# Optimization experiments

Measured on AMD Instinct MI355X. Metric: run time of the kernel, lower is better.

Reference implementation:

```python
import jax, jax.numpy as jnp
import numpy as np

N = 8192
NUM_FEAT = 512
NUM_HIDDENS = 128


def _mlp_params(key, fin, fh):
    k1, k2, k3, k4 = jax.random.split(key, 4)
    s1 = 1.0 / np.sqrt(fin)
    s2 = 1.0 / np.sqrt(fh)
    W1 = jax.random.uniform(k1, (fin, fh), jnp.float32, -s1, s1)
    b1 = jax.random.uniform(k2, (fh,), jnp.float32, -s1, s1)
    W2 = jax.random.uniform(k3, (fh, fh), jnp.float32, -s2, s2)
    b2 = jax.random.uniform(k4, (fh,), jnp.float32, -s2, s2)
    return W1, b1, W2, b2


def setup_inputs() -> dict:
    key = jax.random.key(0)
    ks = jax.random.split(key, 9)
    feat = jax.random.normal(ks[0], (N, NUM_FEAT), jnp.float32)
    adj = jax.random.uniform(ks[1], (N, N), jnp.float32)
    aa = jax.random.uniform(ks[2], (N, N), jnp.float32)
    mod = jax.random.normal(ks[3], (N, N), jnp.float32)
    Wl1, bl1, Wl2, bl2 = _mlp_params(ks[4], NUM_FEAT, NUM_HIDDENS)
    Wu1, bu1, Wu2, bu2 = _mlp_params(ks[5], NUM_FEAT, NUM_HIDDENS)
    Wa1, ba1, Wa2, ba2 = _mlp_params(ks[6], NUM_FEAT, NUM_HIDDENS)
    Wm1, bm1, Wm2, bm2 = _mlp_params(ks[7], NUM_FEAT, NUM_HIDDENS)
    ws = jnp.zeros((3,), jnp.float32)  # nn.init.zeros_(weighted_sum)
    return dict(feat=feat, adj=adj, aa=aa, mod=mod,
                Wl1=Wl1, bl1=bl1, Wl2=Wl2, bl2=bl2,
                Wu1=Wu1, bu1=bu1, Wu2=Wu2, bu2=bu2,
                Wa1=Wa1, ba1=ba1, Wa2=Wa2, ba2=ba2,
                Wm1=Wm1, bm1=bm1, Wm2=Wm2, bm2=bm2,
                ws=ws)


def _latent(feat, W1, b1, W2, b2):
    h = jax.nn.relu(feat @ W1 + b1)
    return h @ W2 + b2  # [N, H]


def reference(feat, adj, aa, mod,
              Wl1, bl1, Wl2, bl2,
              Wu1, bu1, Wu2, bu2,
              Wa1, ba1, Wa2, ba2,
              Wm1, bm1, Wm2, bm2, ws):
    lat_link = _latent(feat, Wl1, bl1, Wl2, bl2)
    lat_aa = _latent(feat, Wa1, ba1, Wa2, ba2)
    lat_mod = _latent(feat, Wm1, bm1, Wm2, bm2)
    lat_unlink = _latent(feat, Wu1, bu1, Wu2, bu2)

    link_ctx = jax.nn.sigmoid(lat_link @ lat_link.T)          # [N, N]
    aa_ctx = jax.nn.sigmoid((lat_aa @ lat_aa.T) * aa)         # [N, N]
    mod_ctx = jax.nn.sigmoid((lat_mod @ lat_mod.T) * mod)     # [N, N]

    w = jax.nn.softmax(ws)  # [3]
    # cat(..., dim=2) @ w  ==  weighted sum of the three contexts
    weight_link = w[0] * link_ctx + w[1] * aa_ctx + w[2] * mod_ctx

    weight_unlink = jax.nn.sigmoid(lat_unlink @ lat_unlink.T)
    return (weight_link - weight_unlink) * adj + weight_unlink
```

## Files before the change

kernel.cpp:

```cpp
#include <hip/hip_runtime.h>


typedef __attribute__((ext_vector_type(8))) short short8;
typedef __attribute__((ext_vector_type(4))) float f32x4;

__device__ __forceinline__ unsigned short f2bf(float x) {
  union { float f; unsigned u; } v; v.f = x;
  unsigned u = v.u + 0x7FFFu + ((v.u >> 16) & 1u);
  return (unsigned short)(u >> 16);
}

__device__ __forceinline__ float sigf(float x) {
  float e = __builtin_amdgcn_exp2f(-1.4426950408889634f * x);
  return __builtin_amdgcn_rcpf(1.0f + e);
}

__device__ __forceinline__ void gload_lds16(const float* g, float* l) {
  __builtin_amdgcn_global_load_lds(
      (const __attribute__((address_space(1))) void*)g,
      (__attribute__((address_space(3))) void*)l, 16, 0, 0);
}

__global__ __launch_bounds__(256) void k_featfrag(const float* __restrict__ feat,
                                                  unsigned short* __restrict__ dst) {
  int t = blockIdx.x * 256 + threadIdx.x;
  int row = t >> 6, kc = t & 63;
  const float4* s = reinterpret_cast<const float4*>(feat + row * 512 + kc * 8);
  float4 v0 = s[0], v1 = s[1];
  short8 o;
  o[0] = f2bf(v0.x); o[1] = f2bf(v0.y); o[2] = f2bf(v0.z); o[3] = f2bf(v0.w);
  o[4] = f2bf(v1.x); o[5] = f2bf(v1.y); o[6] = f2bf(v1.z); o[7] = f2bf(v1.w);
  int mb = row >> 4, kk = kc >> 2;
  int lane = ((kc & 3) << 4) | (row & 15);
  *reinterpret_cast<short8*>(dst + ((size_t)((mb * 16 + kk) * 64 + lane)) * 8) = o;
}

__global__ __launch_bounds__(256) void k_wfrag(
    const float* __restrict__ w1_0, const float* __restrict__ w1_1,
    const float* __restrict__ w1_2, const float* __restrict__ w1_3,
    const float* __restrict__ w2_0, const float* __restrict__ w2_1,
    const float* __restrict__ w2_2, const float* __restrict__ w2_3,
    unsigned short* __restrict__ w1f, unsigned short* __restrict__ w2f) {
  int t = blockIdx.x * 256 + threadIdx.x;
  if (t < 32768) {
    int lane = t & 63, nb = (t >> 6) & 7, kk = (t >> 9) & 15, g = t >> 13;
    const float* W = g == 0 ? w1_0 : g == 1 ? w1_1 : g == 2 ? w1_2 : w1_3;
    int q = lane >> 4, r = lane & 15;
    int col = nb * 16 + r;
    short8 o;
#pragma unroll
    for (int j = 0; j < 8; ++j) o[j] = f2bf(W[(kk * 32 + q * 8 + j) * 128 + col]);
    *reinterpret_cast<short8*>(w1f + (size_t)t * 8) = o;
  } else if (t < 40960) {
    int t2 = t - 32768;
    int lane = t2 & 63, nb = (t2 >> 6) & 7, kk = (t2 >> 9) & 3, g = t2 >> 11;
    const float* W = g == 0 ? w2_0 : g == 1 ? w2_1 : g == 2 ? w2_2 : w2_3;
    int q = lane >> 4, r = lane & 15;
    int col = nb * 16 + r;
    short8 o;
#pragma unroll
    for (int j = 0; j < 8; ++j) o[j] = f2bf(W[(kk * 32 + q * 8 + j) * 128 + col]);
    *reinterpret_cast<short8*>(w2f + (size_t)t2 * 8) = o;
  }
}

__global__ __launch_bounds__(256) void k_gemm1(
    const unsigned short* __restrict__ featf, const unsigned short* __restrict__ w1f,
    const float* __restrict__ b1_0, const float* __restrict__ b1_1,
    const float* __restrict__ b1_2, const float* __restrict__ b1_3,
    unsigned short* __restrict__ hfrag) {
  int bi = blockIdx.x, g = blockIdx.y;
  int lane = threadIdx.x & 63, w = threadIdx.x >> 6;
  int wm = w >> 1, wn = w & 1;
  int q = lane >> 4, r = lane & 15;
  int mbase = 8 * bi + 4 * wm;

  f32x4 s[4][4];
#pragma unroll
  for (int mi = 0; mi < 4; ++mi)
#pragma unroll
    for (int nj = 0; nj < 4; ++nj) s[mi][nj] = (f32x4){0.f, 0.f, 0.f, 0.f};

  for (int kk = 0; kk < 16; ++kk) {
    short8 a[4], b[4];
#pragma unroll
    for (int mi = 0; mi < 4; ++mi)
      a[mi] = *reinterpret_cast<const short8*>(
          featf + ((size_t)(((mbase + mi) * 16 + kk) * 64 + lane)) * 8);
#pragma unroll
    for (int nj = 0; nj < 4; ++nj)
      b[nj] = *reinterpret_cast<const short8*>(
          w1f + ((size_t)(((g * 16 + kk) * 8 + 4 * wn + nj) * 64 + lane)) * 8);
#pragma unroll
    for (int mi = 0; mi < 4; ++mi)
#pragma unroll
      for (int nj = 0; nj < 4; ++nj)
        s[mi][nj] = __builtin_amdgcn_mfma_f32_16x16x32_bf16(a[mi], b[nj], s[mi][nj], 0, 0, 0);
  }

  const float* b1 = g == 0 ? b1_0 : g == 1 ? b1_1 : g == 2 ? b1_2 : b1_3;
#pragma unroll
  for (int nj = 0; nj < 4; ++nj) {
    int cl = 64 * wn + 16 * nj + r;
    float bias = b1[cl];
    int Cg = 128 * g + cl;
    int kkd = Cg >> 5;
    int lane2hi = ((Cg >> 3) & 3) << 4;
    int j2 = Cg & 7;
#pragma unroll
    for (int mi = 0; mi < 4; ++mi) {
#pragma unroll
      for (int v = 0; v < 4; ++v) {
        int R = 128 * bi + 64 * wm + 16 * mi + 4 * q + v;
        float val = fmaxf(s[mi][nj][v] + bias, 0.0f);
        int mb = R >> 4;
        int lane2 = lane2hi | (R & 15);
        hfrag[((size_t)((mb * 16 + kkd) * 64 + lane2)) * 8 + j2] = f2bf(val);
      }
    }
  }
}

__global__ __launch_bounds__(256) void k_gemm2(
    const unsigned short* __restrict__ hfrag, const unsigned short* __restrict__ w2f,
    const float* __restrict__ b2_0, const float* __restrict__ b2_1,
    const float* __restrict__ b2_2, const float* __restrict__ b2_3,
    unsigned short* __restrict__ latf) {
  int bi = blockIdx.x, g = blockIdx.y;
  int lane = threadIdx.x & 63, w = threadIdx.x >> 6;
  int wm = w >> 1, wn = w & 1;
  int q = lane >> 4, r = lane & 15;
  int mbase = 8 * bi + 4 * wm;

  f32x4 s[4][4];
#pragma unroll
  for (int mi = 0; mi < 4; ++mi)
#pragma unroll
    for (int nj = 0; nj < 4; ++nj) s[mi][nj] = (f32x4){0.f, 0.f, 0.f, 0.f};

#pragma unroll
  for (int kk = 0; kk < 4; ++kk) {
    short8 a[4], b[4];
#pragma unroll
    for (int mi = 0; mi < 4; ++mi)
      a[mi] = *reinterpret_cast<const short8*>(
          hfrag + ((size_t)(((mbase + mi) * 16 + 4 * g + kk) * 64 + lane)) * 8);
#pragma unroll
    for (int nj = 0; nj < 4; ++nj)
      b[nj] = *reinterpret_cast<const short8*>(
          w2f + ((size_t)(((g * 4 + kk) * 8 + 4 * wn + nj) * 64 + lane)) * 8);
#pragma unroll
    for (int mi = 0; mi < 4; ++mi)
#pragma unroll
      for (int nj = 0; nj < 4; ++nj)
        s[mi][nj] = __builtin_amdgcn_mfma_f32_16x16x32_bf16(a[mi], b[nj], s[mi][nj], 0, 0, 0);
  }

  const float* b2 = g == 0 ? b2_0 : g == 1 ? b2_1 : g == 2 ? b2_2 : b2_3;
#pragma unroll
  for (int nj = 0; nj < 4; ++nj) {
    int cl = 64 * wn + 16 * nj + r;
    float bias = b2[cl];
    int kkd = cl >> 5;
    int lane2hi = ((cl >> 3) & 3) << 4;
    int j2 = cl & 7;
#pragma unroll
    for (int mi = 0; mi < 4; ++mi) {
#pragma unroll
      for (int v = 0; v < 4; ++v) {
        int R = 128 * bi + 64 * wm + 16 * mi + 4 * q + v;
        float val = s[mi][nj][v] + bias;
        int mb = R >> 4;
        int lane2 = lane2hi | (R & 15);
        latf[((size_t)(((g * 512 + mb) * 4 + kkd) * 64 + lane2)) * 8 + j2] = f2bf(val);
      }
    }
  }
}

__global__ __launch_bounds__(256, 3) void k_ctx(
    const unsigned short* __restrict__ latf,
    const float* __restrict__ adj, const float* __restrict__ aa,
    const float* __restrict__ mod, const float* __restrict__ wsv,
    float* __restrict__ out) {
  __shared__ float smem[2][3][4][256];

  int bid = blockIdx.x;
  int colstrip = bid & 7;
  int rowgrp = bid >> 3;

  int tid = threadIdx.x;
  int lane = tid & 63, w = tid >> 6;
  int q = lane >> 4, r = lane & 15;

  int mbi = rowgrp * 4 + w;
  int mbj0 = colstrip * 64;

  size_t ewoff = (size_t)(mbi * 16 + r) * 8192 + (size_t)colstrip * 1024 + 4 * q;

  float s0w = wsv[0], s1w = wsv[1], s2w = wsv[2];
  float mx = fmaxf(fmaxf(s0w, s1w), s2w);
  float e0 = __builtin_amdgcn_exp2f(1.4426950408889634f * (s0w - mx));
  float e1 = __builtin_amdgcn_exp2f(1.4426950408889634f * (s1w - mx));
  float e2 = __builtin_amdgcn_exp2f(1.4426950408889634f * (s2w - mx));
  float inv = __builtin_amdgcn_rcpf(e0 + e1 + e2);
  float w0 = e0 * inv, w1 = e1 * inv, w2 = e2 * inv;

  const size_t GS = (size_t)512 * 2048;

  short8 fi[4][4];
#pragma unroll
  for (int g = 0; g < 4; ++g)
#pragma unroll
    for (int kk = 0; kk < 4; ++kk) {
      fi[g][kk] = *reinterpret_cast<const short8*>(
          latf + GS * g + (((size_t)mbi * 4 + kk) << 9) + lane * 8);
      asm volatile("" : "+v"(fi[g][kk]));
    }

  gload_lds16(aa + ewoff, &smem[0][0][w][0]);
  gload_lds16(mod + ewoff, &smem[0][1][w][0]);
  gload_lds16(adj + ewoff, &smem[0][2][w][0]);
  asm volatile("s_waitcnt vmcnt(0)" ::: "memory");

  for (int t = 0; t < 64; ++t) {
    int buf = t & 1, nbuf = buf ^ 1;
    const unsigned short* fjb =
        latf + (((size_t)(mbj0 + t) * 4) << 9) + lane * 8;

    short8 fj[4][4];
#pragma unroll
    for (int g = 0; g < 4; ++g)
#pragma unroll
      for (int kk = 0; kk < 4; ++kk)
        fj[g][kk] = *reinterpret_cast<const short8*>(fjb + GS * g + 512 * kk);

    __builtin_amdgcn_sched_barrier(0);
    {
      size_t ewnext = ewoff + (size_t)(t < 63 ? t + 1 : t) * 16;
      gload_lds16(aa + ewnext, &smem[nbuf][0][w][0]);
      gload_lds16(mod + ewnext, &smem[nbuf][1][w][0]);
      gload_lds16(adj + ewnext, &smem[nbuf][2][w][0]);
    }
    asm volatile("s_waitcnt vmcnt(3)" ::: "memory");

    f32x4 sg, o4;

    sg = (f32x4){0.f, 0.f, 0.f, 0.f};
    sg = __builtin_amdgcn_mfma_f32_16x16x32_bf16(fj[0][0], fi[0][0], sg, 0, 0, 0);
    sg = __builtin_amdgcn_mfma_f32_16x16x32_bf16(fj[0][1], fi[0][1], sg, 0, 0, 0);
    sg = __builtin_amdgcn_mfma_f32_16x16x32_bf16(fj[0][2], fi[0][2], sg, 0, 0, 0);
    sg = __builtin_amdgcn_mfma_f32_16x16x32_bf16(fj[0][3], fi[0][3], sg, 0, 0, 0);
#pragma unroll
    for (int v = 0; v < 4; ++v) o4[v] = w0 * sigf(sg[v]);

    sg = (f32x4){0.f, 0.f, 0.f, 0.f};
    sg = __builtin_amdgcn_mfma_f32_16x16x32_bf16(fj[1][0], fi[1][0], sg, 0, 0, 0);
    sg = __builtin_amdgcn_mfma_f32_16x16x32_bf16(fj[1][1], fi[1][1], sg, 0, 0, 0);
    sg = __builtin_amdgcn_mfma_f32_16x16x32_bf16(fj[1][2], fi[1][2], sg, 0, 0, 0);
    sg = __builtin_amdgcn_mfma_f32_16x16x32_bf16(fj[1][3], fi[1][3], sg, 0, 0, 0);
    {
      f32x4 ew = *reinterpret_cast<const f32x4*>(&smem[buf][0][w][lane * 4]);
#pragma unroll
      for (int v = 0; v < 4; ++v) o4[v] += w1 * sigf(sg[v] * ew[v]);
    }

    sg = (f32x4){0.f, 0.f, 0.f, 0.f};
    sg = __builtin_amdgcn_mfma_f32_16x16x32_bf16(fj[2][0], fi[2][0], sg, 0, 0, 0);
    sg = __builtin_amdgcn_mfma_f32_16x16x32_bf16(fj[2][1], fi[2][1], sg, 0, 0, 0);
    sg = __builtin_amdgcn_mfma_f32_16x16x32_bf16(fj[2][2], fi[2][2], sg, 0, 0, 0);
    sg = __builtin_amdgcn_mfma_f32_16x16x32_bf16(fj[2][3], fi[2][3], sg, 0, 0, 0);
    {
      f32x4 ew = *reinterpret_cast<const f32x4*>(&smem[buf][1][w][lane * 4]);
#pragma unroll
      for (int v = 0; v < 4; ++v) o4[v] += w2 * sigf(sg[v] * ew[v]);
    }

    sg = (f32x4){0.f, 0.f, 0.f, 0.f};
    sg = __builtin_amdgcn_mfma_f32_16x16x32_bf16(fj[3][0], fi[3][0], sg, 0, 0, 0);
    sg = __builtin_amdgcn_mfma_f32_16x16x32_bf16(fj[3][1], fi[3][1], sg, 0, 0, 0);
    sg = __builtin_amdgcn_mfma_f32_16x16x32_bf16(fj[3][2], fi[3][2], sg, 0, 0, 0);
    sg = __builtin_amdgcn_mfma_f32_16x16x32_bf16(fj[3][3], fi[3][3], sg, 0, 0, 0);
    {
      f32x4 ew = *reinterpret_cast<const f32x4*>(&smem[buf][2][w][lane * 4]);
      f32x4 res;
#pragma unroll
      for (int v = 0; v < 4; ++v) {
        float u = sigf(sg[v]);
        res[v] = ew[v] * (o4[v] - u) + u;
      }
      __builtin_nontemporal_store(res, reinterpret_cast<f32x4*>(out + ewoff + (size_t)t * 16));
    }
  }
}

extern "C" void kernel_launch(void* const* d_in, const int* in_sizes, int n_in,
                              void* d_out, int out_size, void* d_ws, size_t ws_size,
                              hipStream_t stream) {
  const float* feat = (const float*)d_in[0];
  const float* adj  = (const float*)d_in[1];
  const float* aa   = (const float*)d_in[2];
  const float* mod  = (const float*)d_in[3];
  const float* W1g[4] = {(const float*)d_in[4], (const float*)d_in[12],
                         (const float*)d_in[16], (const float*)d_in[8]};
  const float* b1g[4] = {(const float*)d_in[5], (const float*)d_in[13],
                         (const float*)d_in[17], (const float*)d_in[9]};
  const float* W2g[4] = {(const float*)d_in[6], (const float*)d_in[14],
                         (const float*)d_in[18], (const float*)d_in[10]};
  const float* b2g[4] = {(const float*)d_in[7], (const float*)d_in[15],
                         (const float*)d_in[19], (const float*)d_in[11]};
  const float* wsv = (const float*)d_in[20];
  float* out = (float*)d_out;

  unsigned short* featf = (unsigned short*)d_ws;
  unsigned short* hfrag = featf + 4194304;
  unsigned short* latf  = hfrag + 4194304;
  unsigned short* w1f   = latf + 4194304;
  unsigned short* w2f   = w1f + 262144;
  if (ws_size < 25821184) return;

  k_featfrag<<<2048, 256, 0, stream>>>(feat, featf);
  k_wfrag<<<160, 256, 0, stream>>>(W1g[0], W1g[1], W1g[2], W1g[3],
                                   W2g[0], W2g[1], W2g[2], W2g[3], w1f, w2f);
  k_gemm1<<<dim3(64, 4), 256, 0, stream>>>(featf, w1f, b1g[0], b1g[1], b1g[2], b1g[3], hfrag);
  k_gemm2<<<dim3(64, 4), 256, 0, stream>>>(hfrag, w2f, b2g[0], b2g[1], b2g[2], b2g[3], latf);
  k_ctx<<<1024, 256, 0, stream>>>(latf, adj, aa, mod, wsv, out);
}
```

Before: 448.9 us.

## Restructure ctx kernel: one row block per workgroup, share latent fragments via LDS

Each workgroup of 8 waves now handles a full 16-row strip across all columns. The row-side latent fragments are staged once in LDS instead of held in registers per wave, and the elementwise adj/aa/mod tiles are loaded as contiguous 128-column row chunks. Per-step barriers synchronise the double-buffered LDS prefetch. This makes the elementwise reads and output writes full-row contiguous and frees registers, but it adds LDS reads of the fragments every step, a workgroup barrier per iteration, and output stores that are no longer nontemporal.

```diff
diff --git a/kernel.cpp b/kernel.cpp
--- a/kernel.cpp
+++ b/kernel.cpp
@@ -19,6 +19,25 @@
   __builtin_amdgcn_global_load_lds(
       (const __attribute__((address_space(1))) void*)g,
       (__attribute__((address_space(3))) void*)l, 16, 0, 0);
+}
+__device__ __forceinline__ void gload_lds16u(const unsigned short* g, unsigned short* l) {
+  __builtin_amdgcn_global_load_lds(
+      (const __attribute__((address_space(1))) void*)g,
+      (__attribute__((address_space(3))) void*)l, 16, 0, 0);
+}
+
+__device__ __forceinline__ unsigned lds_off(const void* p) {
+  return (unsigned)(uintptr_t)(const __attribute__((address_space(3))) void*)p;
+}
+__device__ __forceinline__ f32x4 ds_read_f32x4(unsigned a) {
+  f32x4 d;
+  asm volatile("ds_read_b128 %0, %1" : "=v"(d) : "v"(a));
+  return d;
+}
+__device__ __forceinline__ short8 ds_read_frag(unsigned a) {
+  short8 d;
+  asm volatile("ds_read_b128 %0, %1" : "=v"(d) : "v"(a));
+  return d;
 }
 
 __global__ __launch_bounds__(256) void k_featfrag(const float* __restrict__ feat,
@@ -178,25 +197,19 @@
   }
 }
 
-__global__ __launch_bounds__(256, 3) void k_ctx(
+__global__ __launch_bounds__(512, 2) void k_ctx(
     const unsigned short* __restrict__ latf,
     const float* __restrict__ adj, const float* __restrict__ aa,
     const float* __restrict__ mod, const float* __restrict__ wsv,
     float* __restrict__ out) {
-  __shared__ float smem[2][3][4][256];
+  __shared__ unsigned short fi_lds[8192];
+  __shared__ float ew_lds[2][3][2048];
 
   int bid = blockIdx.x;
-  int colstrip = bid & 7;
-  int rowgrp = bid >> 3;
-
   int tid = threadIdx.x;
   int lane = tid & 63, w = tid >> 6;
   int q = lane >> 4, r = lane & 15;
-
-  int mbi = rowgrp * 4 + w;
-  int mbj0 = colstrip * 64;
-
-  size_t ewoff = (size_t)(mbi * 16 + r) * 8192 + (size_t)colstrip * 1024 + 4 * q;
+  int mbi = bid;
 
   float s0w = wsv[0], s1w = wsv[1], s2w = wsv[2];
   float mx = fmaxf(fmaxf(s0w, s1w), s2w);
@@ -208,26 +221,31 @@
 
   const size_t GS = (size_t)512 * 2048;
 
-  short8 fi[4][4];
-#pragma unroll
-  for (int g = 0; g < 4; ++g)
-#pragma unroll
-    for (int kk = 0; kk < 4; ++kk) {
-      fi[g][kk] = *reinterpret_cast<const short8*>(
-          latf + GS * g + (((size_t)mbi * 4 + kk) << 9) + lane * 8);
-      asm volatile("" : "+v"(fi[g][kk]));
-    }
-
-  gload_lds16(aa + ewoff, &smem[0][0][w][0]);
-  gload_lds16(mod + ewoff, &smem[0][1][w][0]);
-  gload_lds16(adj + ewoff, &smem[0][2][w][0]);
+#pragma unroll
+  for (int e = 0; e < 2; ++e) {
+    int i = 2 * w + e;
+    int g = i >> 2, kk = i & 3;
+    gload_lds16u(latf + GS * g + (size_t)(mbi * 4 + kk) * 512 + lane * 8,
+                 &fi_lds[i * 512]);
+  }
+  size_t rowbase = (size_t)(mbi * 16 + 2 * w + (lane >> 5)) * 8192 + (lane & 31) * 4;
+  gload_lds16(aa + rowbase, &ew_lds[0][0][w * 256]);
+  gload_lds16(mod + rowbase, &ew_lds[0][1][w * 256]);
+  gload_lds16(adj + rowbase, &ew_lds[0][2][w * 256]);
   asm volatile("s_waitcnt vmcnt(0)" ::: "memory");
-
-  for (int t = 0; t < 64; ++t) {
-    int buf = t & 1, nbuf = buf ^ 1;
+  __builtin_amdgcn_s_barrier();
+
+  unsigned fib = lds_off(fi_lds);
+  unsigned ewb = lds_off(&ew_lds[0][0][0]);
+  unsigned l16 = (unsigned)lane * 16u;
+  unsigned ewlane = (unsigned)(((r >> 1) * 256 + (r & 1) * 128 + 16 * w + 4 * q) * 4);
+
+#pragma unroll 1
+  for (int s = 0; s < 64; ++s) {
+    int buf = s & 1, nbuf = buf ^ 1;
+
     const unsigned short* fjb =
-        latf + (((size_t)(mbj0 + t) * 4) << 9) + lane * 8;
-
+        latf + (size_t)((s * 8 + w) * 4) * 512 + lane * 8;
     short8 fj[4][4];
 #pragma unroll
     for (int g = 0; g < 4; ++g)
@@ -236,61 +254,97 @@
         fj[g][kk] = *reinterpret_cast<const short8*>(fjb + GS * g + 512 * kk);
 
     __builtin_amdgcn_sched_barrier(0);
-    {
-      size_t ewnext = ewoff + (size_t)(t < 63 ? t + 1 : t) * 16;
-      gload_lds16(aa + ewnext, &smem[nbuf][0][w][0]);
-      gload_lds16(mod + ewnext, &smem[nbuf][1][w][0]);
-      gload_lds16(adj + ewnext, &smem[nbuf][2][w][0]);
-    }
+
+    {
+      int s1 = (s < 63) ? s + 1 : s;
+      size_t fs = rowbase + (size_t)s1 * 128;
+      gload_lds16(aa + fs, &ew_lds[nbuf][0][w * 256]);
+      gload_lds16(mod + fs, &ew_lds[nbuf][1][w * 256]);
+      gload_lds16(adj + fs, &ew_lds[nbuf][2][w * 256]);
+    }
+    __builtin_amdgcn_sched_barrier(0);
     asm volatile("s_waitcnt vmcnt(3)" ::: "memory");
+    __builtin_amdgcn_sched_barrier(0);
+
+    unsigned ewc = ewb + (unsigned)buf * 24576u + ewlane;
+    f32x4 ewa = ds_read_f32x4(ewc);
+    f32x4 ewm = ds_read_f32x4(ewc + 8192u);
+    f32x4 ewj = ds_read_f32x4(ewc + 16384u);
 
     f32x4 sg, o4;
 
-    sg = (f32x4){0.f, 0.f, 0.f, 0.f};
-    sg = __builtin_amdgcn_mfma_f32_16x16x32_bf16(fj[0][0], fi[0][0], sg, 0, 0, 0);
-    sg = __builtin_amdgcn_mfma_f32_16x16x32_bf16(fj[0][1], fi[0][1], sg, 0, 0, 0);
-    sg = __builtin_amdgcn_mfma_f32_16x16x32_bf16(fj[0][2], fi[0][2], sg, 0, 0, 0);
-    sg = __builtin_amdgcn_mfma_f32_16x16x32_bf16(fj[0][3], fi[0][3], sg, 0, 0, 0);
-#pragma unroll
-    for (int v = 0; v < 4; ++v) o4[v] = w0 * sigf(sg[v]);
-
-    sg = (f32x4){0.f, 0.f, 0.f, 0.f};
-    sg = __builtin_amdgcn_mfma_f32_16x16x32_bf16(fj[1][0], fi[1][0], sg, 0, 0, 0);
-    sg = __builtin_amdgcn_mfma_f32_16x16x32_bf16(fj[1][1], fi[1][1], sg, 0, 0, 0);
-    sg = __builtin_amdgcn_mfma_f32_16x16x32_bf16(fj[1][2], fi[1][2], sg, 0, 0, 0);
-    sg = __builtin_amdgcn_mfma_f32_16x16x32_bf16(fj[1][3], fi[1][3], sg, 0, 0, 0);
-    {
-      f32x4 ew = *reinterpret_cast<const f32x4*>(&smem[buf][0][w][lane * 4]);
-#pragma unroll
-      for (int v = 0; v < 4; ++v) o4[v] += w1 * sigf(sg[v] * ew[v]);
-    }
-
-    sg = (f32x4){0.f, 0.f, 0.f, 0.f};
-    sg = __builtin_amdgcn_mfma_f32_16x16x32_bf16(fj[2][0], fi[2][0], sg, 0, 0, 0);
-    sg = __builtin_amdgcn_mfma_f32_16x16x32_bf16(fj[2][1], fi[2][1], sg, 0, 0, 0);
-    sg = __builtin_amdgcn_mfma_f32_16x16x32_bf16(fj[2][2], fi[2][2], sg, 0, 0, 0);
-    sg = __builtin_amdgcn_mfma_f32_16x16x32_bf16(fj[2][3], fi[2][3], sg, 0, 0, 0);
-    {
-      f32x4 ew = *reinterpret_cast<const f32x4*>(&smem[buf][1][w][lane * 4]);
-#pragma unroll
-      for (int v = 0; v < 4; ++v) o4[v] += w2 * sigf(sg[v] * ew[v]);
-    }
-
-    sg = (f32x4){0.f, 0.f, 0.f, 0.f};
-    sg = __builtin_amdgcn_mfma_f32_16x16x32_bf16(fj[3][0], fi[3][0], sg, 0, 0, 0);
-    sg = __builtin_amdgcn_mfma_f32_16x16x32_bf16(fj[3][1], fi[3][1], sg, 0, 0, 0);
-    sg = __builtin_amdgcn_mfma_f32_16x16x32_bf16(fj[3][2], fi[3][2], sg, 0, 0, 0);
-    sg = __builtin_amdgcn_mfma_f32_16x16x32_bf16(fj[3][3], fi[3][3], sg, 0, 0, 0);
-    {
-      f32x4 ew = *reinterpret_cast<const f32x4*>(&smem[buf][2][w][lane * 4]);
+    {
+      short8 f0 = ds_read_frag(fib + 0 * 1024 + l16);
+      short8 f1 = ds_read_frag(fib + 1 * 1024 + l16);
+      short8 f2 = ds_read_frag(fib + 2 * 1024 + l16);
+      short8 f3 = ds_read_frag(fib + 3 * 1024 + l16);
+      asm volatile("s_waitcnt lgkmcnt(0)" ::: "memory");
+      __builtin_amdgcn_sched_barrier(0);
+      sg = (f32x4){0.f, 0.f, 0.f, 0.f};
+      sg = __builtin_amdgcn_mfma_f32_16x16x32_bf16(fj[0][0], f0, sg, 0, 0, 0);
+      sg = __builtin_amdgcn_mfma_f32_16x16x32_bf16(fj[0][1], f1, sg, 0, 0, 0);
+      sg = __builtin_amdgcn_mfma_f32_16x16x32_bf16(fj[0][2], f2, sg, 0, 0, 0);
+      sg = __builtin_amdgcn_mfma_f32_16x16x32_bf16(fj[0][3], f3, sg, 0, 0, 0);
+#pragma unroll
+      for (int v = 0; v < 4; ++v) o4[v] = w0 * sigf(sg[v]);
+    }
+
+    {
+      short8 f0 = ds_read_frag(fib + 4 * 1024 + l16);
+      short8 f1 = ds_read_frag(fib + 5 * 1024 + l16);
+      short8 f2 = ds_read_frag(fib + 6 * 1024 + l16);
+      short8 f3 = ds_read_frag(fib + 7 * 1024 + l16);
+      asm volatile("s_waitcnt lgkmcnt(0)" ::: "memory");
+      __builtin_amdgcn_sched_barrier(0);
+      sg = (f32x4){0.f, 0.f, 0.f, 0.f};
+      sg = __builtin_amdgcn_mfma_f32_16x16x32_bf16(fj[1][0], f0, sg, 0, 0, 0);
+      sg = __builtin_amdgcn_mfma_f32_16x16x32_bf16(fj[1][1], f1, sg, 0, 0, 0);
+      sg = __builtin_amdgcn_mfma_f32_16x16x32_bf16(fj[1][2], f2, sg, 0, 0, 0);
+      sg = __builtin_amdgcn_mfma_f32_16x16x32_bf16(fj[1][3], f3, sg, 0, 0, 0);
+#pragma unroll
+      for (int v = 0; v < 4; ++v) o4[v] += w1 * sigf(sg[v] * ewa[v]);
+    }
+
+    {
+      short8 f0 = ds_read_frag(fib + 8 * 1024 + l16);
+      short8 f1 = ds_read_frag(fib + 9 * 1024 + l16);
+      short8 f2 = ds_read_frag(fib + 10 * 1024 + l16);
+      short8 f3 = ds_read_frag(fib + 11 * 1024 + l16);
+      asm volatile("s_waitcnt lgkmcnt(0)" ::: "memory");
+      __builtin_amdgcn_sched_barrier(0);
+      sg = (f32x4){0.f, 0.f, 0.f, 0.f};
+      sg = __builtin_amdgcn_mfma_f32_16x16x32_bf16(fj[2][0], f0, sg, 0, 0, 0);
+      sg = __builtin_amdgcn_mfma_f32_16x16x32_bf16(fj[2][1], f1, sg, 0, 0, 0);
+      sg = __builtin_amdgcn_mfma_f32_16x16x32_bf16(fj[2][2], f2, sg, 0, 0, 0);
+      sg = __builtin_amdgcn_mfma_f32_16x16x32_bf16(fj[2][3], f3, sg, 0, 0, 0);
+#pragma unroll
+      for (int v = 0; v < 4; ++v) o4[v] += w2 * sigf(sg[v] * ewm[v]);
+    }
+
+    {
+      short8 f0 = ds_read_frag(fib + 12 * 1024 + l16);
+      short8 f1 = ds_read_frag(fib + 13 * 1024 + l16);
+      short8 f2 = ds_read_frag(fib + 14 * 1024 + l16);
+      short8 f3 = ds_read_frag(fib + 15 * 1024 + l16);
+      asm volatile("s_waitcnt lgkmcnt(0)" ::: "memory");
+      __builtin_amdgcn_sched_barrier(0);
+      sg = (f32x4){0.f, 0.f, 0.f, 0.f};
+      sg = __builtin_amdgcn_mfma_f32_16x16x32_bf16(fj[3][0], f0, sg, 0, 0, 0);
+      sg = __builtin_amdgcn_mfma_f32_16x16x32_bf16(fj[3][1], f1, sg, 0, 0, 0);
+      sg = __builtin_amdgcn_mfma_f32_16x16x32_bf16(fj[3][2], f2, sg, 0, 0, 0);
+      sg = __builtin_amdgcn_mfma_f32_16x16x32_bf16(fj[3][3], f3, sg, 0, 0, 0);
       f32x4 res;
 #pragma unroll
       for (int v = 0; v < 4; ++v) {
         float u = sigf(sg[v]);
-        res[v] = ew[v] * (o4[v] - u) + u;
+        res[v] = ewj[v] * (o4[v] - u) + u;
       }
-      __builtin_nontemporal_store(res, reinterpret_cast<f32x4*>(out + ewoff + (size_t)t * 16));
-    }
+      size_t outoff = (size_t)(mbi * 16 + r) * 8192 + s * 128 + 16 * w + 4 * q;
+      *reinterpret_cast<f32x4*>(out + outoff) = res;
+    }
+
+    asm volatile("s_waitcnt vmcnt(1)" ::: "memory");
+    __builtin_amdgcn_s_barrier();
   }
 }
 
@@ -324,5 +378,5 @@
                                    W2g[0], W2g[1], W2g[2], W2g[3], w1f, w2f);
   k_gemm1<<<dim3(64, 4), 256, 0, stream>>>(featf, w1f, b1g[0], b1g[1], b1g[2], b1g[3], hfrag);
   k_gemm2<<<dim3(64, 4), 256, 0, stream>>>(hfrag, w2f, b2g[0], b2g[1], b2g[2], b2g[3], latf);
-  k_ctx<<<1024, 256, 0, stream>>>(latf, adj, aa, mod, wsv, out);
-}
+  k_ctx<<<512, 512, 0, stream>>>(latf, adj, aa, mod, wsv, out);
+}
```

After: 396.9 us. -11.6%, faster.
